# Kernel tuning notes

Measured on AMD Instinct MI355X. Metric: run time of the kernel, lower is better.

## Reference

```python
import jax, jax.numpy as jnp
import numpy as np

B, E, K, P, C = 4096, 8, 4, 96, 32  # samples, experts, top_k, pred_len, channels
EPS = 2.220446049250313e-16  # np.finfo(float).eps, as in the torch code


def setup_inputs() -> dict:
    key = jax.random.key(0)
    k1, k2 = jax.random.split(key)
    # Build sparse top-k gates exactly as the upstream router would: topk + softmax, scattered dense.
    logits = jax.random.normal(k1, (B, E), dtype=jnp.float32)
    top_vals, top_idx = jax.lax.top_k(logits, K)
    top_w = jax.nn.softmax(top_vals, axis=-1)
    gates = jnp.zeros((B, E), dtype=jnp.float32).at[jnp.arange(B)[:, None], top_idx].set(top_w)
    # Dispatch indices: torch does nonzero(gates).sort(0) -> entries grouped by expert.
    mask = np.asarray(gates) > 0
    b_idx, e_idx = np.nonzero(mask)                  # row-major: sorted by batch then expert
    order = np.argsort(e_idx, kind='stable')         # group by expert (== torch.cat over per-expert xs)
    batch_index = jnp.asarray(b_idx[order], dtype=jnp.int64)
    expert_index = jnp.asarray(e_idx[order], dtype=jnp.int64)
    # Stitched expert outputs [N=B*K, P, C]; modest scale since forward applies exp().
    x = jax.random.normal(k2, (B * K, P, C), dtype=jnp.float32) * 0.5
    return {"x": x, "gates": gates, "batch_index": batch_index, "expert_index": expert_index}


def reference(x, gates, batch_index, expert_index):
    # _nonzero_gates = gather(gates[_batch_index], 1, _expert_index)
    nz_gates = gates[batch_index, expert_index]                      # [N]
    # stitched = cat(xs).exp() scaled per-sample by its gate weight
    stitched = jnp.exp(x) * nz_gates[:, None, None]                  # [N, P, C]
    # combined = zeros(B,P,C).index_add(0, batch_index, stitched)
    combined = jnp.zeros((gates.shape[0], x.shape[1], x.shape[2]), dtype=x.dtype)
    combined = combined.at[batch_index].add(stitched)
    # combined[combined == 0] = eps; log
    combined = jnp.where(combined == 0, jnp.asarray(EPS, combined.dtype), combined)
    return jnp.log(combined)
```

## Files before the change

### kernel.cpp

```cpp
#include <hip/hip_runtime.h>

#define BATCH 4096
#define NEXP 8
#define TOPK 4
#define PC 3072
#define EPSV 2.220446049250313e-16f

typedef float f32x4 __attribute__((ext_vector_type(4)));

__global__ __launch_bounds__(256) void build_inv_kernel(
        const int* __restrict__ batch_index,
        const int* __restrict__ expert_index,
        const float* __restrict__ gates,
        int* __restrict__ inv,
        float* __restrict__ gval,
        int N) {
    int n = blockIdx.x * blockDim.x + threadIdx.x;
    if (n >= N) return;
    int b = batch_index[n];
    int e = expert_index[n];
    const float* grow = gates + b * NEXP;
    int slot = 0;
    #pragma unroll
    for (int q = 0; q < NEXP - 1; ++q)
        slot += (q < e && grow[q] > 0.0f) ? 1 : 0;
    inv[b * TOPK + slot]  = n;
    gval[b * TOPK + slot] = grow[e];
}

__global__ __launch_bounds__(256) void combine_kernel(
        const float* __restrict__ x,
        const int* __restrict__ inv,
        const float* __restrict__ gval,
        float* __restrict__ out) {
    const int b = blockIdx.x;
    const int t = threadIdx.x;

    const int   n0 = inv[b * TOPK + 0], n1 = inv[b * TOPK + 1],
                n2 = inv[b * TOPK + 2], n3 = inv[b * TOPK + 3];
    const float g0 = gval[b * TOPK + 0], g1 = gval[b * TOPK + 1],
                g2 = gval[b * TOPK + 2], g3 = gval[b * TOPK + 3];

    const f32x4* x0 = (const f32x4*)(x + (size_t)n0 * PC) + t;
    const f32x4* x1 = (const f32x4*)(x + (size_t)n1 * PC) + t;
    const f32x4* x2 = (const f32x4*)(x + (size_t)n2 * PC) + t;
    const f32x4* x3 = (const f32x4*)(x + (size_t)n3 * PC) + t;
    f32x4* o = (f32x4*)(out + (size_t)b * PC) + t;

    f32x4 a0[3], a1[3], a2[3], a3[3];
    #pragma unroll
    for (int j = 0; j < 3; ++j) {
        a0[j] = x0[j * 256];
        a1[j] = x1[j * 256];
        a2[j] = x2[j * 256];
        a3[j] = x3[j * 256];
    }

    #pragma unroll
    for (int j = 0; j < 3; ++j) {
        f32x4 r;
        #pragma unroll
        for (int c = 0; c < 4; ++c) {
            float s = g0 * __expf(a0[j][c]) + g1 * __expf(a1[j][c])
                    + g2 * __expf(a2[j][c]) + g3 * __expf(a3[j][c]);
            r[c] = __logf(s == 0.0f ? EPSV : s);
        }
        __builtin_nontemporal_store(r, o + j * 256);
    }
}

extern "C" void kernel_launch(void* const* d_in, const int* in_sizes, int n_in,
                              void* d_out, int out_size, void* d_ws, size_t ws_size,
                              hipStream_t stream) {
    const float* x            = (const float*)d_in[0];
    const float* gates        = (const float*)d_in[1];
    const int*   batch_index  = (const int*)d_in[2];
    const int*   expert_index = (const int*)d_in[3];
    float* out = (float*)d_out;
    const int N = in_sizes[2];

    int*   inv  = (int*)d_ws;
    float* gval = (float*)(inv + BATCH * TOPK);

    build_inv_kernel<<<(N + 255) / 256, 256, 0, stream>>>(
        batch_index, expert_index, gates, inv, gval, N);

    combine_kernel<<<BATCH, 256, 0, stream>>>(x, inv, gval, out);
}
```

Before: 45.89 us.

## Fuse inverse-index build into combine kernel via per-block binary search

Removes the separate build_inv kernel and its workspace round-trip. Each block reads its gate row to find active experts, then each wave binary-searches the expert-sorted (expert, batch) key arrays to locate the dispatch index for each of its top-k slots. A ballot-guarded fallback does a linear scan if the search fails. The aim is to save one kernel launch and the global scatter/read of inv/gval. In exchange every wave does a 14-step dependent chain of global loads before the main loads can start, which adds latency.

```diff
diff --git a/kernel.cpp b/kernel.cpp
--- a/kernel.cpp
+++ b/kernel.cpp
@@ -1,4 +1,5 @@
 #include <hip/hip_runtime.h>
+#include <climits>
 
 #define BATCH 4096
 #define NEXP 8
@@ -8,38 +9,73 @@
 
 typedef float f32x4 __attribute__((ext_vector_type(4)));
 
-__global__ __launch_bounds__(256) void build_inv_kernel(
+__global__ __launch_bounds__(256) void fused_combine_kernel(
+        const float* __restrict__ x,
+        const float* __restrict__ gates,
         const int* __restrict__ batch_index,
         const int* __restrict__ expert_index,
-        const float* __restrict__ gates,
-        int* __restrict__ inv,
-        float* __restrict__ gval,
+        float* __restrict__ out,
         int N) {
-    int n = blockIdx.x * blockDim.x + threadIdx.x;
-    if (n >= N) return;
-    int b = batch_index[n];
-    int e = expert_index[n];
+    const int b    = blockIdx.x;
+    const int t    = threadIdx.x;
+    const int lane = t & 63;
+
     const float* grow = gates + b * NEXP;
-    int slot = 0;
+    int   e0 = 0, e1 = 0, e2 = 0, e3 = 0, cnt = 0;
+    float g0 = 0.f, g1 = 0.f, g2 = 0.f, g3 = 0.f;
     #pragma unroll
-    for (int q = 0; q < NEXP - 1; ++q)
-        slot += (q < e && grow[q] > 0.0f) ? 1 : 0;
-    inv[b * TOPK + slot]  = n;
-    gval[b * TOPK + slot] = grow[e];
-}
+    for (int q = 0; q < NEXP; ++q) {
+        float v = grow[q];
+        if (v > 0.0f) {
+            if      (cnt == 0) { e0 = q; g0 = v; }
+            else if (cnt == 1) { e1 = q; g1 = v; }
+            else if (cnt == 2) { e2 = q; g2 = v; }
+            else if (cnt == 3) { e3 = q; g3 = v; }
+            ++cnt;
+        }
+    }
 
-__global__ __launch_bounds__(256) void combine_kernel(
-        const float* __restrict__ x,
-        const int* __restrict__ inv,
-        const float* __restrict__ gval,
-        float* __restrict__ out) {
-    const int b = blockIdx.x;
-    const int t = threadIdx.x;
+    const int   ek = (lane == 0) ? e0 : (lane == 1) ? e1 : (lane == 2) ? e2 : e3;
+    const float gk = (lane == 0) ? g0 : (lane == 1) ? g1 : (lane == 2) ? g2 : g3;
+    const int key  = ek * BATCH + b;
+    int lo = 0, hi = N;
+    for (int it = 0; it < 14; ++it) {
+        int  mid  = (lo + hi) >> 1;
+        int  kmid = expert_index[mid] * BATCH + batch_index[mid];
+        bool less = kmid < key;
+        lo = less ? mid + 1 : lo;
+        hi = less ? hi : mid;
+    }
 
-    const int   n0 = inv[b * TOPK + 0], n1 = inv[b * TOPK + 1],
-                n2 = inv[b * TOPK + 2], n3 = inv[b * TOPK + 3];
-    const float g0 = gval[b * TOPK + 0], g1 = gval[b * TOPK + 1],
-                g2 = gval[b * TOPK + 2], g3 = gval[b * TOPK + 3];
+    int  lov = (lo < N) ? lo : (N - 1);
+    bool ok  = (lane >= TOPK) || (gk == 0.0f) ||
+               (expert_index[lov] == ek && batch_index[lov] == b);
+    if (__ballot(ok) != ~0ULL) {
+        int f0 = INT_MAX, f1 = INT_MAX, f2 = INT_MAX, f3 = INT_MAX;
+        for (int base = lane; base < N; base += 64) {
+            if (batch_index[base] == b) {
+                int em = expert_index[base];
+                if      (em == e0) f0 = base;
+                else if (em == e1) f1 = base;
+                else if (em == e2) f2 = base;
+                else if (em == e3) f3 = base;
+            }
+        }
+        #pragma unroll
+        for (int off = 32; off; off >>= 1) {
+            f0 = min(f0, __shfl_xor(f0, off, 64));
+            f1 = min(f1, __shfl_xor(f1, off, 64));
+            f2 = min(f2, __shfl_xor(f2, off, 64));
+            f3 = min(f3, __shfl_xor(f3, off, 64));
+        }
+        lov = (lane == 0) ? f0 : (lane == 1) ? f1 : (lane == 2) ? f2 : f3;
+    }
+    lov = (lov >= 0 && lov < N) ? lov : 0;
+
+    const int n0 = __shfl(lov, 0, 64);
+    const int n1 = __shfl(lov, 1, 64);
+    const int n2 = __shfl(lov, 2, 64);
+    const int n3 = __shfl(lov, 3, 64);
 
     const f32x4* x0 = (const f32x4*)(x + (size_t)n0 * PC) + t;
     const f32x4* x1 = (const f32x4*)(x + (size_t)n1 * PC) + t;
@@ -78,12 +114,8 @@
     const int*   expert_index = (const int*)d_in[3];
     float* out = (float*)d_out;
     const int N = in_sizes[2];
+    const int B = in_sizes[1] / NEXP;
 
-    int*   inv  = (int*)d_ws;
-    float* gval = (float*)(inv + BATCH * TOPK);
-
-    build_inv_kernel<<<(N + 255) / 256, 256, 0, stream>>>(
-        batch_index, expert_index, gates, inv, gval, N);
-
-    combine_kernel<<<BATCH, 256, 0, stream>>>(x, inv, gval, out);
+    fused_combine_kernel<<<B, 256, 0, stream>>>(
+        x, gates, batch_index, expert_index, out, N);
 }
```

After: 97.65 us. +112.8%, slower.
